# Optimization experiments

Hardware: AMD Instinct MI355X
Metric: run time of the kernel (lower is better)

Reference implementation:

```python
import jax, jax.numpy as jnp
import numpy as np

OUT, IN, GS = 16384, 4096, 16
G = OUT * IN // GS  # 4194304 groups


def setup_inputs() -> dict:
    key = jax.random.key(0)
    k1, k2, k3, k4 = jax.random.split(key, 4)
    x = jax.random.normal(k1, (8, 32, IN), dtype=jnp.float32)
    weight_q2 = jax.random.randint(k2, (G, GS // 4), 0, 256, dtype=jnp.int32)
    weight_norm = jax.random.uniform(k3, (G, 1), dtype=jnp.float16)
    bias = jax.random.normal(k4, (OUT,), dtype=jnp.float32)
    return {"x": x, "weight_q2": weight_q2, "weight_norm": weight_norm, "bias": bias}


def _dequant_2bit(weight_q2, weight_norm):
    # torch: xq_out[:, i::4] = (xq >> 2i) & 3  =>  element index within group = i + 4*k
    # where k = packed column (slow, stride 4), i = shift index (fast).
    norm = weight_norm.astype(jnp.float32)                      # [G, 1]
    shifts = jnp.arange(4, dtype=jnp.int32) * 2                 # [4]
    vals = (weight_q2[:, :, None] >> shifts) & 3                # [G, 4(pack k), 4(shift i)]
    xq_out = vals.astype(jnp.float32).reshape(G, GS)            # [G, 16], layout k*4 + i
    w = (xq_out / 3.0) * (2.0 * norm) - norm                    # [G, 16]
    return w.reshape(OUT, IN)


def reference(x, weight_q2, weight_norm, bias):
    w = _dequant_2bit(weight_q2, weight_norm)                   # [OUT, IN] fp32
    return jnp.einsum('bsi,oi->bso', x, w) + bias
```

## Files before the change

### kernel.cpp

```cpp
#include <hip/hip_runtime.h>
#include <stdint.h>

#define M_DIM 256
#define N_DIM 16384
#define K_DIM 4096
#define BN 64
#define BK 64
#define NT (K_DIM / BK)

typedef __bf16 bf16x8 __attribute__((ext_vector_type(8)));
typedef float  f32x4  __attribute__((ext_vector_type(4)));

__device__ __forceinline__ uint32_t f2bf(float f) {
  uint32_t u = __float_as_uint(f);
  return (u + 0x7fffu + ((u >> 16) & 1u)) >> 16;
}

#define LDS_BARRIER() \
  asm volatile("s_waitcnt lgkmcnt(0)\n\ts_barrier" ::: "memory")

__global__ __launch_bounds__(256) void cvt_x_kernel(const float* __restrict__ x,
                                                    uint4* __restrict__ ws) {
  int T = blockIdx.x * 256 + threadIdx.x;
  int mb_glob = T >> 13;
  int r       = T & 8191;
  int kch     = r >> 6;
  int L       = r & 63;
  int row = mb_glob * 16 + (L & 15);
  int k   = kch * 32 + (L >> 4) * 8;
  const float* p = x + (size_t)row * K_DIM + k;
  float4 a = *(const float4*)p;
  float4 b = *(const float4*)(p + 4);
  uint4 o;
  o.x = f2bf(a.x) | (f2bf(a.y) << 16);
  o.y = f2bf(a.z) | (f2bf(a.w) << 16);
  o.z = f2bf(b.x) | (f2bf(b.y) << 16);
  o.w = f2bf(b.z) | (f2bf(b.w) << 16);
  ws[T] = o;
}

__device__ __forceinline__ uint4 deq8(uint2 q, float nv) {
  float a2 = nv * (2.0f / 3.0f);
  uint32_t tlo = f2bf(-nv) | (f2bf(fmaf(1.0f, a2, -nv)) << 16);
  uint32_t thi = f2bf(fmaf(2.0f, a2, -nv)) | (f2bf(fmaf(3.0f, a2, -nv)) << 16);
  uint32_t s0 = ((q.x & 3u) | ((q.x & 0xCu) << 14)) * 0x0202u + 0x01000100u;
  uint32_t s1 = (((q.x >> 4) & 3u) | ((q.x & 0xC0u) << 10)) * 0x0202u + 0x01000100u;
  uint32_t s2 = ((q.y & 3u) | ((q.y & 0xCu) << 14)) * 0x0202u + 0x01000100u;
  uint32_t s3 = (((q.y >> 4) & 3u) | ((q.y & 0xC0u) << 10)) * 0x0202u + 0x01000100u;
  uint4 r;
  r.x = __builtin_amdgcn_perm(thi, tlo, s0);
  r.y = __builtin_amdgcn_perm(thi, tlo, s1);
  r.z = __builtin_amdgcn_perm(thi, tlo, s2);
  r.w = __builtin_amdgcn_perm(thi, tlo, s3);
  return r;
}

__global__ __launch_bounds__(512, 4) void gemm2bit_kernel(
    const uint4*    __restrict__ aws,
    const uint32_t* __restrict__ q2,
    const float*    __restrict__ nrm,
    const float*    __restrict__ bias,
    float*          __restrict__ out)
{
  __shared__ uint4 Bb[2][512];

  const int tid  = threadIdx.x;
  const int lane = tid & 63;
  const int w    = tid >> 6;
  const int wm   = w >> 1;
  const int wn   = w & 1;
  const int lo4  = lane & 15;
  const int qd   = lane >> 4;
  const int n0   = blockIdx.x * BN;
  const int m0   = blockIdx.y * 128;

  const int lrs = lane ^ qd;

  const int nloc = tid >> 3;
  const int kg   = (tid >> 1) & 3;
  const int h    = tid & 1;
  const int grow = n0 + nloc;
  const int qd2   = (kg & 1) * 2 + h;
  const int bslot = ((kg >> 1) * 4 + (nloc >> 4)) * 64 + qd2 * 16 +
                    ((nloc & 15) ^ qd2);

  const uint4* pA = aws + ((size_t)(blockIdx.y * 8 + wm * 2) * 128) * 64 + lane;
  const uint32_t* pq = q2 + ((size_t)grow * 256 + kg) * 4 + h * 2;
  const float*    pn = nrm + (size_t)grow * 256 + kg;

  f32x4 acc[2][2];
#pragma unroll
  for (int s = 0; s < 2; ++s)
#pragma unroll
    for (int u = 0; u < 2; ++u)
      acc[s][u] = (f32x4){0.f, 0.f, 0.f, 0.f};

  uint4 af0[4], af1[4];
  uint2 qA, qB;
  float nA, nB;

#pragma unroll
  for (int s = 0; s < 2; ++s)
#pragma unroll
    for (int ts = 0; ts < 2; ++ts)
      af0[s * 2 + ts] = pA[(size_t)s * 8192 + ts * 64];
  uint2 q0 = *(const uint2*)pq;
  float n0v = pn[0];
  qA = *(const uint2*)(pq + 16);
  nA = pn[4];
  qB = *(const uint2*)(pq + 32);
  nB = pn[8];
  Bb[0][bslot] = deq8(q0, n0v);
  LDS_BARRIER();

#define GEMM_BODY(T, PR, AFC, AFN, QC, NC)                                      \
  do {                                                                          \
    if ((T) + 1 < NT) {                                                         \
      size_t toff = (size_t)((T) + 1) * 128;                                    \
      _Pragma("unroll")                                                         \
      for (int s = 0; s < 2; ++s)                                               \
        _Pragma("unroll")                                                       \
        for (int ts = 0; ts < 2; ++ts)                                          \
          AFN[s * 2 + ts] = pA[(size_t)s * 8192 + toff + ts * 64];              \
    }                                                                           \
    _Pragma("unroll")                                                           \
    for (int ts = 0; ts < 2; ++ts) {                                            \
      bf16x8 bfv[2];                                                            \
      _Pragma("unroll")                                                         \
      for (int u = 0; u < 2; ++u)                                               \
        bfv[u] = *(const bf16x8*)&Bb[PR][(ts * 4 + wn * 2 + u) * 64 + lrs];     \
      _Pragma("unroll")                                                         \
      for (int s = 0; s < 2; ++s) {                                             \
        bf16x8 av = __builtin_bit_cast(bf16x8, AFC[s * 2 + ts]);                \
        _Pragma("unroll")                                                       \
        for (int u = 0; u < 2; ++u)                                             \
          acc[s][u] = __builtin_amdgcn_mfma_f32_16x16x32_bf16(av, bfv[u],       \
                                                              acc[s][u], 0, 0, 0);\
      }                                                                         \
    }                                                                           \
    if ((T) + 1 < NT) Bb[(PR) ^ 1][bslot] = deq8(QC, NC);                       \
    if ((T) + 3 < NT) {                                                         \
      QC = *(const uint2*)(pq + (size_t)((T) + 3) * 16);                        \
      NC = pn[(size_t)((T) + 3) * 4];                                           \
    }                                                                           \
    LDS_BARRIER();                                                              \
  } while (0)

  for (int t2 = 0; t2 < NT; t2 += 2) {
    GEMM_BODY(t2,     0, af0, af1, qA, nA);
    GEMM_BODY(t2 + 1, 1, af1, af0, qB, nB);
  }
#undef GEMM_BODY

  float bv[2];
#pragma unroll
  for (int u = 0; u < 2; ++u)
    bv[u] = bias[n0 + wn * 32 + u * 16 + lo4];

#pragma unroll
  for (int s = 0; s < 2; ++s) {
    int mrow = m0 + wm * 32 + s * 16 + qd * 4;
#pragma unroll
    for (int u = 0; u < 2; ++u) {
      int ncol = n0 + wn * 32 + u * 16 + lo4;
      float* p = out + (size_t)mrow * N_DIM + ncol;
#pragma unroll
      for (int r = 0; r < 4; ++r)
        p[(size_t)r * N_DIM] = acc[s][u][r] + bv[u];
    }
  }
}

extern "C" void kernel_launch(void* const* d_in, const int* in_sizes, int n_in,
                              void* d_out, int out_size, void* d_ws, size_t ws_size,
                              hipStream_t stream) {
  const float*    x    = (const float*)d_in[0];
  const uint32_t* q2   = (const uint32_t*)d_in[1];
  const float*    nm   = (const float*)d_in[2];
  const float*    bias = (const float*)d_in[3];
  float*          out  = (float*)d_out;
  uint4*          aws  = (uint4*)d_ws;

  cvt_x_kernel<<<512, 256, 0, stream>>>(x, aws);
  gemm2bit_kernel<<<dim3(N_DIM / BN, 2), 512, 0, stream>>>(aws, q2, nm, bias, out);
}
```

Baseline: 166.7 us.

## Split block into producer waves for dequant and consumer waves for MFMA

Warp-specializes the GEMM block: waves 0-3 only load activations and run MFMAs over the full 64-column tile with raised scheduling priority, while waves 4-7 only load packed 2-bit weights, dequantize them and write them to LDS. Each producer lane now handles a full 16-byte weight chunk and computes the norm lookup table once for two outputs. The aim is to overlap dequant ALU work with matrix math and cut redundant LUT computation. In exchange, half the waves do no MFMA work, so each consumer wave carries twice the accumulators and its register pressure rises.

```diff
diff --git a/kernel.cpp b/kernel.cpp
--- a/kernel.cpp
+++ b/kernel.cpp
@@ -39,14 +39,12 @@
   ws[T] = o;
 }
 
-__device__ __forceinline__ uint4 deq8(uint2 q, float nv) {
-  float a2 = nv * (2.0f / 3.0f);
-  uint32_t tlo = f2bf(-nv) | (f2bf(fmaf(1.0f, a2, -nv)) << 16);
-  uint32_t thi = f2bf(fmaf(2.0f, a2, -nv)) | (f2bf(fmaf(3.0f, a2, -nv)) << 16);
-  uint32_t s0 = ((q.x & 3u) | ((q.x & 0xCu) << 14)) * 0x0202u + 0x01000100u;
-  uint32_t s1 = (((q.x >> 4) & 3u) | ((q.x & 0xC0u) << 10)) * 0x0202u + 0x01000100u;
-  uint32_t s2 = ((q.y & 3u) | ((q.y & 0xCu) << 14)) * 0x0202u + 0x01000100u;
-  uint32_t s3 = (((q.y >> 4) & 3u) | ((q.y & 0xC0u) << 10)) * 0x0202u + 0x01000100u;
+__device__ __forceinline__ uint4 deq8(uint32_t qx, uint32_t qy, uint32_t tlo,
+                                      uint32_t thi) {
+  uint32_t s0 = ((qx & 3u) | ((qx & 0xCu) << 14)) * 0x0202u + 0x01000100u;
+  uint32_t s1 = (((qx >> 4) & 3u) | ((qx & 0xC0u) << 10)) * 0x0202u + 0x01000100u;
+  uint32_t s2 = ((qy & 3u) | ((qy & 0xCu) << 14)) * 0x0202u + 0x01000100u;
+  uint32_t s3 = (((qy >> 4) & 3u) | ((qy & 0xC0u) << 10)) * 0x0202u + 0x01000100u;
   uint4 r;
   r.x = __builtin_amdgcn_perm(thi, tlo, s0);
   r.y = __builtin_amdgcn_perm(thi, tlo, s1);
@@ -67,107 +65,134 @@
   const int tid  = threadIdx.x;
   const int lane = tid & 63;
   const int w    = tid >> 6;
-  const int wm   = w >> 1;
-  const int wn   = w & 1;
   const int lo4  = lane & 15;
   const int qd   = lane >> 4;
   const int n0   = blockIdx.x * BN;
   const int m0   = blockIdx.y * 128;
 
-  const int lrs = lane ^ qd;
-
-  const int nloc = tid >> 3;
-  const int kg   = (tid >> 1) & 3;
-  const int h    = tid & 1;
-  const int grow = n0 + nloc;
-  const int qd2   = (kg & 1) * 2 + h;
-  const int bslot = ((kg >> 1) * 4 + (nloc >> 4)) * 64 + qd2 * 16 +
-                    ((nloc & 15) ^ qd2);
-
-  const uint4* pA = aws + ((size_t)(blockIdx.y * 8 + wm * 2) * 128) * 64 + lane;
-  const uint32_t* pq = q2 + ((size_t)grow * 256 + kg) * 4 + h * 2;
-  const float*    pn = nrm + (size_t)grow * 256 + kg;
-
-  f32x4 acc[2][2];
-#pragma unroll
-  for (int s = 0; s < 2; ++s)
-#pragma unroll
-    for (int u = 0; u < 2; ++u)
-      acc[s][u] = (f32x4){0.f, 0.f, 0.f, 0.f};
-
-  uint4 af0[4], af1[4];
-  uint2 qA, qB;
-  float nA, nB;
-
-#pragma unroll
-  for (int s = 0; s < 2; ++s)
-#pragma unroll
-    for (int ts = 0; ts < 2; ++ts)
-      af0[s * 2 + ts] = pA[(size_t)s * 8192 + ts * 64];
-  uint2 q0 = *(const uint2*)pq;
-  float n0v = pn[0];
-  qA = *(const uint2*)(pq + 16);
-  nA = pn[4];
-  qB = *(const uint2*)(pq + 32);
-  nB = pn[8];
-  Bb[0][bslot] = deq8(q0, n0v);
-  LDS_BARRIER();
-
-#define GEMM_BODY(T, PR, AFC, AFN, QC, NC)                                      \
-  do {                                                                          \
-    if ((T) + 1 < NT) {                                                         \
-      size_t toff = (size_t)((T) + 1) * 128;                                    \
+  if (w < 4) {
+    const int cw  = w;
+    const int lrs = lane ^ qd;
+
+    const uint4* pA = aws + (size_t)(blockIdx.y * 8 + cw * 2) * 8192 + lane;
+
+    f32x4 acc[2][4];
+#pragma unroll
+    for (int s = 0; s < 2; ++s)
+#pragma unroll
+      for (int u = 0; u < 4; ++u)
+        acc[s][u] = (f32x4){0.f, 0.f, 0.f, 0.f};
+
+    uint4 afE[4], afO[4];
+#pragma unroll
+    for (int s = 0; s < 2; ++s)
+#pragma unroll
+      for (int ts = 0; ts < 2; ++ts)
+        afE[s * 2 + ts] = pA[(size_t)s * 8192 + ts * 64];
+    LDS_BARRIER();
+
+#define CONS_BODY(T, PR, AFC, AFN)                                              \
+    do {                                                                        \
+      if ((T) + 1 < NT) {                                                       \
+        size_t toff = (size_t)((T) + 1) * 128;                                  \
+        _Pragma("unroll")                                                       \
+        for (int s = 0; s < 2; ++s)                                             \
+          _Pragma("unroll")                                                     \
+          for (int ts = 0; ts < 2; ++ts)                                        \
+            AFN[s * 2 + ts] = pA[(size_t)s * 8192 + toff + ts * 64];            \
+      }                                                                         \
+      __builtin_amdgcn_s_setprio(1);                                            \
       _Pragma("unroll")                                                         \
-      for (int s = 0; s < 2; ++s)                                               \
+      for (int ts = 0; ts < 2; ++ts) {                                          \
+        bf16x8 bfv[4];                                                          \
         _Pragma("unroll")                                                       \
-        for (int ts = 0; ts < 2; ++ts)                                          \
-          AFN[s * 2 + ts] = pA[(size_t)s * 8192 + toff + ts * 64];              \
-    }                                                                           \
-    _Pragma("unroll")                                                           \
-    for (int ts = 0; ts < 2; ++ts) {                                            \
-      bf16x8 bfv[2];                                                            \
-      _Pragma("unroll")                                                         \
-      for (int u = 0; u < 2; ++u)                                               \
-        bfv[u] = *(const bf16x8*)&Bb[PR][(ts * 4 + wn * 2 + u) * 64 + lrs];     \
-      _Pragma("unroll")                                                         \
-      for (int s = 0; s < 2; ++s) {                                             \
-        bf16x8 av = __builtin_bit_cast(bf16x8, AFC[s * 2 + ts]);                \
+        for (int u = 0; u < 4; ++u)                                             \
+          bfv[u] = *(const bf16x8*)&Bb[PR][(ts * 4 + u) * 64 + lrs];            \
         _Pragma("unroll")                                                       \
-        for (int u = 0; u < 2; ++u)                                             \
-          acc[s][u] = __builtin_amdgcn_mfma_f32_16x16x32_bf16(av, bfv[u],       \
-                                                              acc[s][u], 0, 0, 0);\
-      }                                                                         \
-    }                                                                           \
-    if ((T) + 1 < NT) Bb[(PR) ^ 1][bslot] = deq8(QC, NC);                       \
-    if ((T) + 3 < NT) {                                                         \
-      QC = *(const uint2*)(pq + (size_t)((T) + 3) * 16);                        \
-      NC = pn[(size_t)((T) + 3) * 4];                                           \
-    }                                                                           \
-    LDS_BARRIER();                                                              \
-  } while (0)
-
-  for (int t2 = 0; t2 < NT; t2 += 2) {
-    GEMM_BODY(t2,     0, af0, af1, qA, nA);
-    GEMM_BODY(t2 + 1, 1, af1, af0, qB, nB);
-  }
-#undef GEMM_BODY
-
-  float bv[2];
-#pragma unroll
-  for (int u = 0; u < 2; ++u)
-    bv[u] = bias[n0 + wn * 32 + u * 16 + lo4];
-
-#pragma unroll
-  for (int s = 0; s < 2; ++s) {
-    int mrow = m0 + wm * 32 + s * 16 + qd * 4;
-#pragma unroll
-    for (int u = 0; u < 2; ++u) {
-      int ncol = n0 + wn * 32 + u * 16 + lo4;
-      float* p = out + (size_t)mrow * N_DIM + ncol;
-#pragma unroll
-      for (int r = 0; r < 4; ++r)
-        p[(size_t)r * N_DIM] = acc[s][u][r] + bv[u];
-    }
+        for (int s = 0; s < 2; ++s) {                                           \
+          bf16x8 av = __builtin_bit_cast(bf16x8, AFC[s * 2 + ts]);              \
+          _Pragma("unroll")                                                     \
+          for (int u = 0; u < 4; ++u)                                           \
+            acc[s][u] = __builtin_amdgcn_mfma_f32_16x16x32_bf16(av, bfv[u],     \
+                                                            acc[s][u], 0, 0, 0);\
+        }                                                                       \
+      }                                                                         \
+      __builtin_amdgcn_s_setprio(0);                                            \
+      LDS_BARRIER();                                                            \
+    } while (0)
+
+    for (int t2 = 0; t2 < NT; t2 += 2) {
+      CONS_BODY(t2,     0, afE, afO);
+      CONS_BODY(t2 + 1, 1, afO, afE);
+    }
+#undef CONS_BODY
+
+    float bv[4];
+#pragma unroll
+    for (int u = 0; u < 4; ++u)
+      bv[u] = bias[n0 + u * 16 + lo4];
+#pragma unroll
+    for (int s = 0; s < 2; ++s) {
+      int mrow = m0 + cw * 32 + s * 16 + qd * 4;
+#pragma unroll
+      for (int u = 0; u < 4; ++u) {
+        int ncol = n0 + u * 16 + lo4;
+        float* p = out + (size_t)mrow * N_DIM + ncol;
+#pragma unroll
+        for (int r = 0; r < 4; ++r)
+          p[(size_t)r * N_DIM] = acc[s][u][r] + bv[u];
+      }
+    }
+  } else {
+    const int pw    = w - 4;
+    const int kg    = lane & 3;
+    const int n_loc = lane >> 2;
+    const int grow  = n0 + pw * 16 + n_loc;
+    const int qd2a  = (kg & 1) * 2;
+    const int qd2b  = qd2a + 1;
+    const int bsA = ((kg >> 1) * 4 + pw) * 64 + qd2a * 16 + (n_loc ^ qd2a);
+    const int bsB = ((kg >> 1) * 4 + pw) * 64 + qd2b * 16 + (n_loc ^ qd2b);
+
+    const uint32_t* pq = q2 + ((size_t)grow * 256 + kg) * 4;
+    const float*    pn = nrm + (size_t)grow * 256 + kg;
+
+    uint4 q0 = *(const uint4*)pq;
+    float y0 = pn[0];
+    uint4 qE = *(const uint4*)(pq + 16);
+    float nE = pn[4];
+    uint4 qO = *(const uint4*)(pq + 32);
+    float nO = pn[8];
+    {
+      float a2 = y0 * (2.0f / 3.0f);
+      uint32_t tlo = f2bf(-y0) | (f2bf(fmaf(1.0f, a2, -y0)) << 16);
+      uint32_t thi = f2bf(fmaf(2.0f, a2, -y0)) | (f2bf(fmaf(3.0f, a2, -y0)) << 16);
+      Bb[0][bsA] = deq8(q0.x, q0.y, tlo, thi);
+      Bb[0][bsB] = deq8(q0.z, q0.w, tlo, thi);
+    }
+    LDS_BARRIER();
+
+#define PROD_BODY(T, PR, QQ, NN)                                                \
+    do {                                                                        \
+      if ((T) + 1 < NT) {                                                       \
+        float a2 = NN * (2.0f / 3.0f);                                          \
+        uint32_t tlo = f2bf(-NN) | (f2bf(fmaf(1.0f, a2, -NN)) << 16);           \
+        uint32_t thi = f2bf(fmaf(2.0f, a2, -NN)) |                              \
+                       (f2bf(fmaf(3.0f, a2, -NN)) << 16);                       \
+        Bb[(PR) ^ 1][bsA] = deq8(QQ.x, QQ.y, tlo, thi);                         \
+        Bb[(PR) ^ 1][bsB] = deq8(QQ.z, QQ.w, tlo, thi);                         \
+      }                                                                         \
+      if ((T) + 3 < NT) {                                                       \
+        QQ = *(const uint4*)(pq + (size_t)((T) + 3) * 16);                      \
+        NN = pn[(size_t)((T) + 3) * 4];                                         \
+      }                                                                         \
+      LDS_BARRIER();                                                            \
+    } while (0)
+
+    for (int t2 = 0; t2 < NT; t2 += 2) {
+      PROD_BODY(t2,     0, qE, nE);
+      PROD_BODY(t2 + 1, 1, qO, nO);
+    }
+#undef PROD_BODY
   }
 }
 
```

Result: faster. 153.9 us (-7.7%).
